# Kernel optimization log

Measured on AMD Instinct MI355X. Metric: run time of the kernel, lower is better.

## Reference

```python
import jax, jax.numpy as jnp
import numpy as np

LOG_2PI = float(np.log(2.0 * np.pi))
EPS = 1e-10


def setup_inputs() -> dict:
    key = jax.random.key(0)
    k1, k2, k3, k4, k5 = jax.random.split(key, 5)
    N, B, C, V = 32768, 32, 32, 16
    x = jax.random.normal(k1, (N, 6), dtype=jnp.float32)
    vote_6d = jax.random.normal(k2, (B, C, V, 6), dtype=jnp.float32)
    scales = jax.random.uniform(k3, (B, C, V), dtype=jnp.float32)
    log_pres = jax.random.normal(k4, (B, C, V), dtype=jnp.float32)
    batch = jnp.sort(jax.random.randint(k5, (N,), 0, B, dtype=jnp.int64))
    return {"x": x, "vote_6d": vote_6d, "scales": scales, "log_pres": log_pres, "batch": batch}


def reference(x, vote_6d, scales, log_pres, batch):
    # x: [N, 6]; vote_6d: [B, C, V, 6]; scales/log_pres: [B, C, V]; batch: [N]
    B = vote_6d.shape[0]
    safe_scale = jnp.clip(scales, EPS)                 # clamp(scale, min=eps)
    mu = vote_6d[batch]                                # [N, C, V, 6] gather by batch idx
    s = safe_scale[batch][..., None]                   # [N, C, V, 1] broadcast over 6 dims
    prior = log_pres[batch]                            # [N, C, V]
    xe = x[:, None, None, :]                           # [N, 1, 1, 6]
    z = (xe - mu) / s
    # Normal log-prob per dim, summed over the 6 pose dims
    vote_log_prob = jnp.sum(-0.5 * z * z - jnp.log(s) - 0.5 * LOG_2PI, axis=-1)  # [N, C, V]
    posterior_logits = prior + vote_log_prob           # [N, C, V]
    N = posterior_logits.shape[0]
    log_prob_per_point = jax.nn.logsumexp(posterior_logits.reshape(N, -1), axis=-1)  # [N]
    log_prob_per_example = jax.ops.segment_sum(log_prob_per_point, batch, num_segments=B)  # [B]
    log_prob_batch = jnp.mean(log_prob_per_example)
    return log_prob_batch, log_prob_per_example
```

## Files before the change

kernel.cpp:

```cpp
#include <hip/hip_runtime.h>
#include <math.h>

#define LOG_2PI_F 1.8378770664093453f
#define EPS_F 1e-10f
#define NB 32
#define CV 512
#define PPW 4
#define KPL 8

__global__ __launch_bounds__(256)
__attribute__((amdgpu_waves_per_eu(2, 4)))
void capsule_main(
    const float* __restrict__ x,
    const float* __restrict__ vote,
    const float* __restrict__ scales,
    const float* __restrict__ log_pres,
    const int* __restrict__ batch,
    float* __restrict__ out_pe,
    float* __restrict__ wsum,
    int n_pts)
{
    const int tid  = threadIdx.x;
    const int lane = tid & 63;
    const int wloc = __builtin_amdgcn_readfirstlane(tid >> 6);
    const int wave = blockIdx.x * 4 + wloc;
    const int p0   = wave * PPW;
    if (p0 >= n_pts) return;

    int pidx = p0 + (lane & (PPW - 1));
    if (pidx >= n_pts) pidx = n_pts - 1;
    const int  pbq     = batch[pidx];
    const int  b0      = __builtin_amdgcn_readfirstlane(pbq);
    const bool uniform = (__ballot(pbq == b0) == ~0ull);

    float a0[KPL], a1[KPL], a2[KPL], a3[KPL], a4[KPL], a5[KPL];
    float ainv[KPL], acoef[KPL];

    auto load_params = [&](int b) {
        #pragma unroll
        for (int j = 0; j < KPL; ++j) {
            const int c = b * CV + lane + 64 * j;
            float s   = fmaxf(scales[c], EPS_F);
            float inv = 1.0f / s;
            const float2* mu2 = (const float2*)(vote + (size_t)c * 6);
            float2 m01 = mu2[0], m23 = mu2[1], m45 = mu2[2];
            a0[j] = m01.x * inv;
            a1[j] = m01.y * inv;
            a2[j] = m23.x * inv;
            a3[j] = m23.y * inv;
            a4[j] = m45.x * inv;
            a5[j] = m45.y * inv;
            ainv[j]  = inv;
            acoef[j] = log_pres[c] - 6.0f * __logf(s) - 3.0f * LOG_2PI_F;
        }
    };

    load_params(b0);

    auto logits = [&](const float* xv, float* l) {
        #pragma unroll
        for (int j = 0; j < KPL; ++j) {
            float z, acc;
            z = fmaf(xv[0], ainv[j], -a0[j]); acc = z * z;
            z = fmaf(xv[1], ainv[j], -a1[j]); acc = fmaf(z, z, acc);
            z = fmaf(xv[2], ainv[j], -a2[j]); acc = fmaf(z, z, acc);
            z = fmaf(xv[3], ainv[j], -a3[j]); acc = fmaf(z, z, acc);
            z = fmaf(xv[4], ainv[j], -a4[j]); acc = fmaf(z, z, acc);
            z = fmaf(xv[5], ainv[j], -a5[j]); acc = fmaf(z, z, acc);
            l[j] = fmaf(acc, -0.5f, acoef[j]);
        }
    };

    auto local_max = [](const float* l) {
        return fmaxf(fmaxf(fmaxf(l[0], l[1]), fmaxf(l[2], l[3])),
                     fmaxf(fmaxf(l[4], l[5]), fmaxf(l[6], l[7])));
    };

    if (uniform && p0 + PPW <= n_pts) {
        float xx[PPW][6];
        #pragma unroll
        for (int q = 0; q < PPW; ++q) {
            const float* xp = x + (size_t)(p0 + q) * 6;
            #pragma unroll
            for (int d = 0; d < 6; ++d) xx[q][d] = xp[d];
        }

        float wavesum = 0.0f;
        #pragma unroll
        for (int q = 0; q < PPW; q += 2) {
            float la[KPL], lb[KPL];
            logits(xx[q],     la);
            logits(xx[q + 1], lb);

            float ma = local_max(la);
            float mb = local_max(lb);
            #pragma unroll
            for (int off = 1; off <= 32; off <<= 1) {
                float ta = __shfl_xor(ma, off, 64);
                float tb = __shfl_xor(mb, off, 64);
                ma = fmaxf(ma, ta);
                mb = fmaxf(mb, tb);
            }

            float ea = (__expf(la[0] - ma) + __expf(la[1] - ma))
                     + (__expf(la[2] - ma) + __expf(la[3] - ma))
                     + (__expf(la[4] - ma) + __expf(la[5] - ma))
                     + (__expf(la[6] - ma) + __expf(la[7] - ma));
            float eb = (__expf(lb[0] - mb) + __expf(lb[1] - mb))
                     + (__expf(lb[2] - mb) + __expf(lb[3] - mb))
                     + (__expf(lb[4] - mb) + __expf(lb[5] - mb))
                     + (__expf(lb[6] - mb) + __expf(lb[7] - mb));
            #pragma unroll
            for (int off = 1; off <= 32; off <<= 1) {
                float ta = __shfl_xor(ea, off, 64);
                float tb = __shfl_xor(eb, off, 64);
                ea += ta;
                eb += tb;
            }

            wavesum += (ma + __logf(ea)) + (mb + __logf(eb));
        }
        if (lane == 0) wsum[wave] = wavesum;
    } else {
        if (lane == 0) wsum[wave] = 0.0f;
        int cur_b = b0;
        for (int q = 0; q < PPW; ++q) {
            const int p = p0 + q;
            if (p >= n_pts) break;
            const int pb = batch[p];
            if (pb != cur_b) { load_params(pb); cur_b = pb; }
            float xv[6];
            const float* xp = x + (size_t)p * 6;
            #pragma unroll
            for (int d = 0; d < 6; ++d) xv[d] = xp[d];
            float l[KPL];
            logits(xv, l);
            float lm = local_max(l);
            #pragma unroll
            for (int off = 1; off <= 32; off <<= 1)
                lm = fmaxf(lm, __shfl_xor(lm, off, 64));
            float es = 0.0f;
            #pragma unroll
            for (int j = 0; j < KPL; ++j) es += __expf(l[j] - lm);
            #pragma unroll
            for (int off = 1; off <= 32; off <<= 1)
                es += __shfl_xor(es, off, 64);
            float lp = lm + __logf(es);
            if (lane == 0) atomicAdd(&out_pe[cur_b], lp);
        }
    }
}

__global__ __launch_bounds__(1024) void final_kernel(
    const float* __restrict__ wsum,
    const int* __restrict__ batch,
    float* __restrict__ d_out,
    int n_waves, int n_pts)
{
    __shared__ float part[NB];
    const int t = threadIdx.x;
    if (t < NB) part[t] = 0.0f;
    __syncthreads();

    for (int w = t; w < n_waves; w += 1024) {
        float s = wsum[w];
        int   pi = w * PPW;
        if (pi >= n_pts) pi = n_pts - 1;
        atomicAdd(&part[batch[pi]], s);
    }
    __syncthreads();

    if (t < 64) {
        float v = 0.0f;
        if (t < NB) {
            v = d_out[1 + t] + part[t];
            d_out[1 + t] = v;
        }
        #pragma unroll
        for (int off = 32; off >= 1; off >>= 1) v += __shfl_xor(v, off, 64);
        if (t == 0) d_out[0] = v * (1.0f / NB);
    }
}

extern "C" void kernel_launch(void* const* d_in, const int* in_sizes, int n_in,
                              void* d_out, int out_size, void* d_ws, size_t ws_size,
                              hipStream_t stream) {
    const float* x        = (const float*)d_in[0];
    const float* vote     = (const float*)d_in[1];
    const float* scales   = (const float*)d_in[2];
    const float* log_pres = (const float*)d_in[3];
    const int*   batch    = (const int*)d_in[4];
    float* out = (float*)d_out;
    float* ws  = (float*)d_ws;

    int n_pts   = in_sizes[0] / 6;
    int n_waves = (n_pts + PPW - 1) / PPW;

    hipMemsetAsync(d_out, 0, (size_t)out_size * sizeof(float), stream);

    int n_blocks = (n_waves + 3) / 4;
    capsule_main<<<n_blocks, 256, 0, stream>>>(x, vote, scales, log_pres, batch,
                                               out + 1, ws, n_pts);

    final_kernel<<<1, 1024, 0, stream>>>(ws, batch, out, n_waves, n_pts);
}
```

Before: 99.18 us.

## Stage per-block batch parameters in LDS and double points per wave

Each block now cooperatively loads the vote, scale and log-prior parameters for its batch into shared memory with coalesced float4 loads. Waves in the uniform path build their per-lane coefficients from LDS instead of issuing strided global loads. Points per wave go from four to eight, which halves the grid and amortizes parameter setup over more points. In exchange every block adds a __syncthreads and about 10KB of LDS, which can limit occupancy. Waves whose batch differs from the block's batch fall back to global loads.

```diff
diff --git a/kernel.cpp b/kernel.cpp
--- a/kernel.cpp
+++ b/kernel.cpp
@@ -5,7 +5,8 @@
 #define EPS_F 1e-10f
 #define NB 32
 #define CV 512
-#define PPW 4
+#define PPW 8
+#define PPB 32
 #define KPL 8
 
 __global__ __launch_bounds__(256)
@@ -20,23 +21,63 @@
     float* __restrict__ wsum,
     int n_pts)
 {
+    __shared__ float s_vote[CV * 6];
+    __shared__ float s_sc[CV];
+    __shared__ float s_lp[CV];
+
     const int tid  = threadIdx.x;
     const int lane = tid & 63;
     const int wloc = __builtin_amdgcn_readfirstlane(tid >> 6);
     const int wave = blockIdx.x * 4 + wloc;
     const int p0   = wave * PPW;
+
+    int pblk = blockIdx.x * PPB;
+    if (pblk >= n_pts) pblk = n_pts - 1;
+    const int bblk = batch[pblk];
+    {
+        const float4* gv = (const float4*)(vote + (size_t)bblk * CV * 6);
+        float4* sv = (float4*)s_vote;
+        #pragma unroll
+        for (int i = 0; i < 3; ++i)
+            sv[tid + 256 * i] = gv[tid + 256 * i];
+        const float4* gs = (const float4*)(scales + (size_t)bblk * CV);
+        const float4* gl = (const float4*)(log_pres + (size_t)bblk * CV);
+        if (tid < 128) {
+            ((float4*)s_sc)[tid] = gs[tid];
+            ((float4*)s_lp)[tid] = gl[tid];
+        }
+    }
+    __syncthreads();
+
     if (p0 >= n_pts) return;
 
     int pidx = p0 + (lane & (PPW - 1));
     if (pidx >= n_pts) pidx = n_pts - 1;
     const int  pbq     = batch[pidx];
     const int  b0      = __builtin_amdgcn_readfirstlane(pbq);
-    const bool uniform = (__ballot(pbq == b0) == ~0ull);
+    const bool uniform = (__ballot(pbq == b0) == ~0ull) && (b0 == bblk);
 
     float a0[KPL], a1[KPL], a2[KPL], a3[KPL], a4[KPL], a5[KPL];
     float ainv[KPL], acoef[KPL];
 
-    auto load_params = [&](int b) {
+    auto build_from_lds = [&]() {
+        #pragma unroll
+        for (int j = 0; j < KPL; ++j) {
+            const int c = lane + 64 * j;
+            float s   = fmaxf(s_sc[c], EPS_F);
+            float inv = 1.0f / s;
+            const float* mu = s_vote + c * 6;
+            a0[j] = mu[0] * inv;
+            a1[j] = mu[1] * inv;
+            a2[j] = mu[2] * inv;
+            a3[j] = mu[3] * inv;
+            a4[j] = mu[4] * inv;
+            a5[j] = mu[5] * inv;
+            ainv[j]  = inv;
+            acoef[j] = s_lp[c] - 6.0f * __logf(s) - 3.0f * LOG_2PI_F;
+        }
+    };
+    auto build_from_global = [&](int b) {
         #pragma unroll
         for (int j = 0; j < KPL; ++j) {
             const int c = b * CV + lane + 64 * j;
@@ -55,8 +96,6 @@
         }
     };
 
-    load_params(b0);
-
     auto logits = [&](const float* xv, float* l) {
         #pragma unroll
         for (int j = 0; j < KPL; ++j) {
@@ -70,13 +109,14 @@
             l[j] = fmaf(acc, -0.5f, acoef[j]);
         }
     };
-
     auto local_max = [](const float* l) {
         return fmaxf(fmaxf(fmaxf(l[0], l[1]), fmaxf(l[2], l[3])),
                      fmaxf(fmaxf(l[4], l[5]), fmaxf(l[6], l[7])));
     };
 
     if (uniform && p0 + PPW <= n_pts) {
+        build_from_lds();
+
         float xx[PPW][6];
         #pragma unroll
         for (int q = 0; q < PPW; ++q) {
@@ -123,12 +163,12 @@
         if (lane == 0) wsum[wave] = wavesum;
     } else {
         if (lane == 0) wsum[wave] = 0.0f;
-        int cur_b = b0;
+        int cur_b = -1;
         for (int q = 0; q < PPW; ++q) {
             const int p = p0 + q;
             if (p >= n_pts) break;
             const int pb = batch[p];
-            if (pb != cur_b) { load_params(pb); cur_b = pb; }
+            if (pb != cur_b) { build_from_global(pb); cur_b = pb; }
             float xv[6];
             const float* xp = x + (size_t)p * 6;
             #pragma unroll
@@ -198,7 +238,7 @@
 
     hipMemsetAsync(d_out, 0, (size_t)out_size * sizeof(float), stream);
 
-    int n_blocks = (n_waves + 3) / 4;
+    int n_blocks = (n_pts + PPB - 1) / PPB;
     capsule_main<<<n_blocks, 256, 0, stream>>>(x, vote, scales, log_pres, batch,
                                                out + 1, ws, n_pts);
 
```

Result: faster. 92.51 us (-6.7%).
